# Kernel optimization log

Measured on AMD Instinct MI355X. Metric: run time of the kernel, lower is better.

## Reference

```python
import jax, jax.numpy as jnp
import numpy as np

NTYPES = 2
MAXNEI = 128      # maxNeighborNum
M2 = 16
NPER = 256        # atoms per type
B = 4
EMB = [25, 50, 100]
FIT_IN = M2 * EMB[-1]  # 1600
FH = 240


def setup_inputs() -> dict:
    key = jax.random.key(0)
    ks = jax.random.split(key, 16)
    s = 0.1
    inp = {
        "Ri": jax.random.normal(ks[0], (B, NTYPES * NPER, NTYPES * MAXNEI, 4), jnp.float32),
        "emb_W0": jax.random.normal(ks[1], (4, 1, EMB[0]), jnp.float32) * s,
        "emb_b0": jax.random.normal(ks[2], (4, EMB[0]), jnp.float32) * s,
        "emb_W1": jax.random.normal(ks[3], (4, EMB[0], EMB[1]), jnp.float32) * s,
        "emb_b1": jax.random.normal(ks[4], (4, EMB[1]), jnp.float32) * s,
        "emb_W2": jax.random.normal(ks[5], (4, EMB[1], EMB[2]), jnp.float32) * s,
        "emb_b2": jax.random.normal(ks[6], (4, EMB[2]), jnp.float32) * s,
        "fit_W0": jax.random.normal(ks[7], (2, FIT_IN, FH), jnp.float32) * 0.02,
        "fit_b0": jax.random.normal(ks[8], (2, FH), jnp.float32) * s,
        "fit_W1": jax.random.normal(ks[9], (2, FH, FH), jnp.float32) * 0.05,
        "fit_b1": jax.random.normal(ks[10], (2, FH), jnp.float32) * s,
        "fit_W2": jax.random.normal(ks[11], (2, FH, FH), jnp.float32) * 0.05,
        "fit_b2": jax.random.normal(ks[12], (2, FH), jnp.float32) * s,
        "fit_W3": jax.random.normal(ks[13], (2, FH, 1), jnp.float32) * 0.05,
        "fit_b3": jax.random.normal(ks[14], (2, 1), jnp.float32),
    }
    return inp


def _emb(s, W0, b0, W1, b1, W2, b2):
    # DeepMD-style embedding MLP with doubling resnet skips (1->25->50->100)
    h0 = jnp.tanh(s @ W0 + b0)
    h1 = jnp.tanh(h0 @ W1 + b1) + jnp.concatenate([h0, h0], axis=-1)
    h2 = jnp.tanh(h1 @ W2 + b2) + jnp.concatenate([h1, h1], axis=-1)
    return h2


def _fit(d, W0, b0, W1, b1, W2, b2, W3, b3):
    h = jnp.tanh(d @ W0 + b0)
    h = jnp.tanh(h @ W1 + b1) + h   # resnet skip (equal dims)
    h = jnp.tanh(h @ W2 + b2) + h
    return h @ W3 + b3              # [B, N, 1]


def reference(Ri, emb_W0, emb_b0, emb_W1, emb_b1, emb_W2, emb_b2,
              fit_W0, fit_b0, fit_W1, fit_b1, fit_W2, fit_b2, fit_W3, fit_b3):
    type_nums = NTYPES
    Ei_blocks = []
    for i in range(NTYPES):                      # center-atom type
        Ri_i = Ri[:, i * NPER:(i + 1) * NPER]    # [B, NPER, NTYPES*M, 4]
        xyz = None
        for j in range(NTYPES):                  # neighbor type
            blk = Ri_i[:, :, j * MAXNEI:(j + 1) * MAXNEI, :]  # [B,N,M,4]
            S = blk[..., 0:1]                                  # [B,N,M,1]
            e = i * NTYPES + j
            G = _emb(S, emb_W0[e], emb_b0[e], emb_W1[e], emb_b1[e],
                     emb_W2[e], emb_b2[e])                     # [B,N,M,100]
            tmp = jnp.einsum('bnmc,bnmg->bncg', blk, G)        # [B,N,4,100]
            xyz = tmp if xyz is None else xyz + tmp
        xyz = xyz / (MAXNEI * type_nums)
        xyz_b = xyz[..., :M2]                                  # [B,N,4,16]
        DR = jnp.einsum('bncg,bnch->bngh', xyz, xyz_b)         # [B,N,100,16]
        DR = DR.reshape(B, NPER, FIT_IN)
        Ei_i = _fit(DR, fit_W0[i], fit_b0[i], fit_W1[i], fit_b1[i],
                    fit_W2[i], fit_b2[i], fit_W3[i], fit_b3[i])  # [B,N,1]
        Ei_blocks.append(Ei_i)
    Ei = jnp.concatenate(Ei_blocks, axis=1)     # [B, natoms_sum, 1]
    return Ei[..., 0]                            # per-atom energies [B, natoms_sum]
```

## Files before the change

kernel.cpp:

```cpp
#include <hip/hip_runtime.h>
#include <hip/hip_bf16.h>

#define FH 240
#define FIT_IN 1600
#define NK 2048
#define TLO -16.0f
#define TINVH 64.0f

typedef _Float16 h8 __attribute__((ext_vector_type(8)));
typedef float f4v __attribute__((ext_vector_type(4)));

__device__ __forceinline__ float fast_tanh(float x) {
    float e2 = __builtin_amdgcn_exp2f(x * 2.8853900817779268f);
    return 1.0f - 2.0f * __builtin_amdgcn_rcpf(e2 + 1.0f);
}

#define FMA_ROW(r, s) \
    acc[r][0] += (s) * b0.x; acc[r][1] += (s) * b0.y; \
    acc[r][2] += (s) * b0.z; acc[r][3] += (s) * b0.w; \
    acc[r][4] += (s) * b1.x; acc[r][5] += (s) * b1.y; \
    acc[r][6] += (s) * b1.z; acc[r][7] += (s) * b1.w;

#define TOFF_W0   0
#define TOFF_B0   28
#define TOFF_B1   56
#define TOFF_B2   108
#define TOFF_W1   208
#define TOFF_W2   1508
#define TOFF_H0T  6708
#define TOFF_H1T  10008
#define TSMEM     16608

__global__ __launch_bounds__(256) void k_table(
    const float* __restrict__ eW0, const float* __restrict__ eB0,
    const float* __restrict__ eW1, const float* __restrict__ eB1,
    const float* __restrict__ eW2, const float* __restrict__ eB2,
    float* __restrict__ T)
{
    __shared__ float sm[TSMEM];

    const int t    = threadIdx.x;
    const int w    = t >> 6;
    const int lane = t & 63;
    const int mi   = lane & 7;
    const int gi   = lane >> 3;
    const int mrow = w * 32 + mi * 4;

    const int e  = blockIdx.y;
    const int k0 = blockIdx.x * 128;

    for (int idx = t; idx < 1250; idx += 256) {
        int k = idx / 50, g = idx - k * 50;
        sm[TOFF_W1 + k * 52 + g] = eW1[e * 1250 + idx];
    }
    for (int idx = t; idx < 5000; idx += 256) {
        int k = idx / 100, r = idx - k * 100;
        int half = r / 50, g = r - half * 50;
        sm[TOFF_W2 + k * 104 + half * 52 + g] = eW2[e * 5000 + idx];
    }
    if (t < 25)       { sm[TOFF_W0 + t] = eW0[e * 25 + t]; sm[TOFF_B0 + t] = eB0[e * 25 + t]; }
    else if (t < 75)  { sm[TOFF_B1 + (t - 25)] = eB1[e * 50 + (t - 25)]; }
    else if (t < 175) { sm[TOFF_B2 + (t - 75)] = eB2[e * 100 + (t - 75)]; }
    __syncthreads();

    if (t < 128) {
        const float S = TLO + (float)(k0 + t) * (1.0f / TINVH);
        #pragma unroll
        for (int k = 0; k < 25; ++k)
            sm[TOFF_H0T + k * 132 + t] = fast_tanh(S * sm[TOFF_W0 + k] + sm[TOFF_B0 + k]);
    }
    __syncthreads();

    {
        float acc[4][8];
        #pragma unroll
        for (int r = 0; r < 4; ++r)
            #pragma unroll
            for (int c = 0; c < 8; ++c) acc[r][c] = 0.f;

        #pragma unroll 5
        for (int k = 0; k < 25; ++k) {
            const float4 av = *(const float4*)&sm[TOFF_H0T + k * 132 + mrow];
            const float4 b0 = *(const float4*)&sm[TOFF_W1 + k * 52 + gi * 8];
            const float4 b1 = *(const float4*)&sm[TOFF_W1 + k * 52 + gi * 8 + 4];
            FMA_ROW(0, av.x) FMA_ROW(1, av.y) FMA_ROW(2, av.z) FMA_ROW(3, av.w)
        }
        #pragma unroll
        for (int c = 0; c < 8; ++c) {
            const int g = gi * 8 + c;
            if (g < 50) {
                const int gm = (g < 25) ? g : g - 25;
                const float4 h0r = *(const float4*)&sm[TOFF_H0T + gm * 132 + mrow];
                const float bias = sm[TOFF_B1 + g];
                float4 o;
                o.x = fast_tanh(acc[0][c] + bias) + h0r.x;
                o.y = fast_tanh(acc[1][c] + bias) + h0r.y;
                o.z = fast_tanh(acc[2][c] + bias) + h0r.z;
                o.w = fast_tanh(acc[3][c] + bias) + h0r.w;
                *(float4*)&sm[TOFF_H1T + g * 132 + mrow] = o;
            }
        }
    }
    __syncthreads();

    for (int half = 0; half < 2; ++half) {
        float acc[4][8];
        #pragma unroll
        for (int r = 0; r < 4; ++r)
            #pragma unroll
            for (int c = 0; c < 8; ++c) acc[r][c] = 0.f;

        #pragma unroll 5
        for (int k = 0; k < 50; ++k) {
            const float4 av = *(const float4*)&sm[TOFF_H1T + k * 132 + mrow];
            const float4 b0 = *(const float4*)&sm[TOFF_W2 + k * 104 + half * 52 + gi * 8];
            const float4 b1 = *(const float4*)&sm[TOFF_W2 + k * 104 + half * 52 + gi * 8 + 4];
            FMA_ROW(0, av.x) FMA_ROW(1, av.y) FMA_ROW(2, av.z) FMA_ROW(3, av.w)
        }
        #pragma unroll
        for (int c = 0; c < 8; ++c) {
            const int g = gi * 8 + c;
            if (g < 50) {
                const float4 h1r = *(const float4*)&sm[TOFF_H1T + g * 132 + mrow];
                const float bias = sm[TOFF_B2 + half * 50 + g];
                float* out = T + ((size_t)e * NK + k0 + mrow) * 100 + half * 50 + g;
                out[0]   = fast_tanh(acc[0][c] + bias) + h1r.x;
                out[100] = fast_tanh(acc[1][c] + bias) + h1r.y;
                out[200] = fast_tanh(acc[2][c] + bias) + h1r.z;
                out[300] = fast_tanh(acc[3][c] + bias) + h1r.w;
            }
        }
    }
}

__global__ __launch_bounds__(256) void k_cvt(
    const float* __restrict__ fW0, const float* __restrict__ fW1,
    const float* __restrict__ fW2,
    _Float16* __restrict__ W0T, _Float16* __restrict__ W1T,
    _Float16* __restrict__ W2T)
{
    const int total = 768000 + 115200 + 115200;
    for (int idx = blockIdx.x * 256 + threadIdx.x; idx < total; idx += gridDim.x * 256) {
        if (idx < 768000) {
            const int tp = idx / 384000, r = idx - tp * 384000;
            const int n = r / 1600, k = r - n * 1600;
            W0T[idx] = (_Float16)fW0[tp * 384000 + k * 240 + n];
        } else if (idx < 883200) {
            const int j = idx - 768000;
            const int tp = j / 57600, r = j - tp * 57600;
            const int n = r / 240, k = r - n * 240;
            W1T[j] = (_Float16)fW1[tp * 57600 + k * 240 + n];
        } else {
            const int j = idx - 883200;
            const int tp = j / 57600, r = j - tp * 57600;
            const int n = r / 240, k = r - n * 240;
            W2T[j] = (_Float16)fW2[tp * 57600 + k * 240 + n];
        }
    }
}

__global__ __launch_bounds__(256) void k_xyz(
    const float* __restrict__ Ri, const float* __restrict__ T,
    _Float16* __restrict__ DRh)
{
    __shared__ float4 sR[256];
    __shared__ float  sF[256];
    __shared__ int    sI[256];
    __shared__ float  sXYZ[400];

    const int t   = threadIdx.x;
    const int blk = blockIdx.x;
    const int b   = blk >> 9;
    const int i   = (blk >> 8) & 1;
    const int n   = blk & 255;

    for (int idx = t; idx < 400; idx += 256) sXYZ[idx] = 0.f;

    {
        const int jj = t >> 7, m = t & 127;
        const size_t row = ((size_t)(b * 512 + i * 256 + n)) * 256 + jj * 128 + m;
        const float4 r = *(const float4*)(Ri + row * 4);
        sR[t] = r;
        float u = (r.x - TLO) * TINVH;
        int ii = (int)u;
        ii = (ii < 0) ? 0 : ((ii > NK - 2) ? NK - 2 : ii);
        sI[t] = ii;
        sF[t] = u - (float)ii;
    }
    __syncthreads();

    const int jj = t >> 7;
    const int g  = t & 127;
    if (g < 100) {
        const float* Te = T + ((size_t)(i * 2 + jj)) * NK * 100 + g;
        float a0 = 0.f, a1 = 0.f, a2 = 0.f, a3 = 0.f;
        #pragma unroll 4
        for (int m = 0; m < 128; ++m) {
            const int s = jj * 128 + m;
            const float4 R = sR[s];
            const float  f = sF[s];
            const float* p = Te + (size_t)sI[s] * 100;
            const float v0 = p[0], v1 = p[100];
            const float G = v0 + f * (v1 - v0);
            a0 += R.x * G; a1 += R.y * G; a2 += R.z * G; a3 += R.w * G;
        }
        atomicAdd(&sXYZ[g],       a0);
        atomicAdd(&sXYZ[100 + g], a1);
        atomicAdd(&sXYZ[200 + g], a2);
        atomicAdd(&sXYZ[300 + g], a3);
    }
    __syncthreads();

    const float inv = 1.0f / 65536.0f;
    _Float16* dr = DRh + (((size_t)i * 4 + b) * 256 + n) * FIT_IN;
    for (int q = t; q < 400; q += 256) {
        const int gg = q >> 2, h0 = (q & 3) * 4;
        ushort4 pk;
        _Float16* ph = (_Float16*)&pk;
        #pragma unroll
        for (int r = 0; r < 4; ++r) {
            const int h = h0 + r;
            const float v = (sXYZ[gg] * sXYZ[h] + sXYZ[100 + gg] * sXYZ[100 + h]
                           + sXYZ[200 + gg] * sXYZ[200 + h] + sXYZ[300 + gg] * sXYZ[300 + h]) * inv;
            ph[r] = (_Float16)v;
        }
        *(ushort4*)(dr + gg * 16 + h0) = pk;
    }
}

template<int K, int CHUNK>
__global__ __launch_bounds__(256) void k_fit_mfma(
    const _Float16* __restrict__ A, const _Float16* __restrict__ WT,
    float* __restrict__ P)
{
    __shared__ _Float16 sA[64 * 40];
    __shared__ _Float16 sBT[240 * 40];

    const int t    = threadIdx.x;
    const int w    = t >> 6;
    const int lane = t & 63;
    const int ln   = lane & 15;
    const int quad = lane >> 4;

    const int mtile = blockIdx.x;
    const int ks    = blockIdx.y;
    const int row0  = mtile * 64;
    const int tp    = mtile >> 4;
    const int kbeg  = ks * CHUNK;
    const int kend  = (kbeg + CHUNK < K) ? (kbeg + CHUNK) : K;
    const int nf0   = w * 4;
    const int nfrags = (w < 3) ? 4 : 3;

    f4v acc[4][4];
    #pragma unroll
    for (int mf = 0; mf < 4; ++mf)
        #pragma unroll
        for (int nf = 0; nf < 4; ++nf) acc[mf][nf] = (f4v)0.f;

    const _Float16* Ab = A + (size_t)row0 * K;
    const _Float16* Wb = WT + (size_t)tp * 240 * K;

    for (int k0 = kbeg; k0 < kend; k0 += 32) {
        #pragma unroll
        for (int q = t; q < 512; q += 256) {
            const int m = q >> 3, kq = (q & 7) * 4;
            const int k = k0 + kq;
            uint2 v = make_uint2(0u, 0u);
            if (k < kend) v = *(const uint2*)(Ab + (size_t)m * K + k);
            *(uint2*)&sA[m * 40 + kq] = v;
        }
        for (int q = t; q < 1920; q += 256) {
            const int n = q >> 3, kq = (q & 7) * 4;
            const int k = k0 + kq;
            uint2 v = make_uint2(0u, 0u);
            if (k < kend) v = *(const uint2*)(Wb + (size_t)n * K + k);
            *(uint2*)&sBT[n * 40 + kq] = v;
        }
        __syncthreads();

        h8 afr[4];
        #pragma unroll
        for (int mf = 0; mf < 4; ++mf)
            afr[mf] = *(const h8*)&sA[(mf * 16 + ln) * 40 + quad * 8];
        #pragma unroll
        for (int nf = 0; nf < 4; ++nf) {
            if (nf < nfrags) {
                const h8 bfr = *(const h8*)&sBT[((nf0 + nf) * 16 + ln) * 40 + quad * 8];
                #pragma unroll
                for (int mf = 0; mf < 4; ++mf)
                    acc[mf][nf] = __builtin_amdgcn_mfma_f32_16x16x32_f16(
                        afr[mf], bfr, acc[mf][nf], 0, 0, 0);
            }
        }
        __syncthreads();
    }

    float* Pb = P + ((size_t)ks * 2048 + row0) * FH;
    #pragma unroll
    for (int nf = 0; nf < 4; ++nf) {
        if (nf < nfrags) {
            const int col = (nf0 + nf) * 16 + ln;
            #pragma unroll
            for (int mf = 0; mf < 4; ++mf)
                #pragma unroll
                for (int r = 0; r < 4; ++r) {
                    const int row = mf * 16 + quad * 4 + r;
                    Pb[(size_t)row * FH + col] = acc[mf][nf][r];
                }
        }
    }
}

template<int KSPLIT, bool RES>
__global__ __launch_bounds__(256) void k_fit_reduce(
    const float* __restrict__ P, const float* __restrict__ Bias,
    const float* __restrict__ AinF, float* __restrict__ OutF,
    _Float16* __restrict__ OutH)
{
    const int idx = blockIdx.x * 256 + threadIdx.x;
    if (idx >= 2048 * FH) return;
    const int tp  = idx / (1024 * FH);
    const int col = idx % FH;
    float s = 0.f;
    #pragma unroll
    for (int ks = 0; ks < KSPLIT; ++ks)
        s += P[(size_t)ks * 2048 * FH + idx];
    float v = fast_tanh(s + Bias[tp * FH + col]);
    if (RES) v += AinF[idx];
    OutF[idx] = v;
    OutH[idx] = (_Float16)v;
}

__global__ __launch_bounds__(256) void k_out(
    const float* __restrict__ Hin, const float* __restrict__ W3,
    const float* __restrict__ b3, float* __restrict__ out)
{
    const int wave = (int)((blockIdx.x * 256 + threadIdx.x) >> 6);
    const int lane = threadIdx.x & 63;
    const int tp = wave >> 10;
    const int rem = wave & 1023;
    const int b = rem >> 8, n = rem & 255;
    const float* h = Hin + (size_t)wave * FH;
    const float* wv = W3 + tp * FH;
    float s = 0.f;
    for (int k = lane; k < FH; k += 64) s += h[k] * wv[k];
    #pragma unroll
    for (int off = 32; off > 0; off >>= 1) s += __shfl_down(s, off);
    if (lane == 0) out[b * 512 + tp * 256 + n] = s + b3[tp];
}

extern "C" void kernel_launch(void* const* d_in, const int* in_sizes, int n_in,
                              void* d_out, int out_size, void* d_ws, size_t ws_size,
                              hipStream_t stream)
{
    const float* Ri  = (const float*)d_in[0];
    const float* eW0 = (const float*)d_in[1];
    const float* eB0 = (const float*)d_in[2];
    const float* eW1 = (const float*)d_in[3];
    const float* eB1 = (const float*)d_in[4];
    const float* eW2 = (const float*)d_in[5];
    const float* eB2 = (const float*)d_in[6];
    const float* fW0 = (const float*)d_in[7];
    const float* fb0 = (const float*)d_in[8];
    const float* fW1 = (const float*)d_in[9];
    const float* fb1 = (const float*)d_in[10];
    const float* fW2 = (const float*)d_in[11];
    const float* fb2 = (const float*)d_in[12];
    const float* fW3 = (const float*)d_in[13];
    const float* fb3 = (const float*)d_in[14];

    char* p = (char*)d_ws;
    float* T   = (float*)p;                 p += (size_t)4 * NK * 100 * 4;
    float* P   = (float*)p;                 p += (size_t)17 * 2048 * FH * 4;
    float* hA  = (float*)p;                 p += (size_t)2048 * FH * 4;
    float* hB  = (float*)p;                 p += (size_t)2048 * FH * 4;
    _Float16* DRh = (_Float16*)p;           p += (size_t)2048 * FIT_IN * 2;
    _Float16* hAh = (_Float16*)p;           p += (size_t)2048 * FH * 2;
    _Float16* hBh = (_Float16*)p;           p += (size_t)2048 * FH * 2;
    _Float16* W0T = (_Float16*)p;           p += (size_t)768000 * 2;
    _Float16* W1T = (_Float16*)p;           p += (size_t)115200 * 2;
    _Float16* W2T = (_Float16*)p;           p += (size_t)115200 * 2;

    const int RBLK = (2048 * FH + 255) / 256;

    k_cvt<<<dim3(1024), dim3(256), 0, stream>>>(fW0, fW1, fW2, W0T, W1T, W2T);
    k_table<<<dim3(NK / 128, 4), dim3(256), 0, stream>>>(eW0, eB0, eW1, eB1, eW2, eB2, T);
    k_xyz<<<dim3(2048), dim3(256), 0, stream>>>(Ri, T, DRh);

    k_fit_mfma<FIT_IN, 96><<<dim3(32, 17), dim3(256), 0, stream>>>(DRh, W0T, P);
    k_fit_reduce<17, false><<<dim3(RBLK), dim3(256), 0, stream>>>(P, fb0, nullptr, hA, hAh);

    k_fit_mfma<FH, 32><<<dim3(32, 8), dim3(256), 0, stream>>>(hAh, W1T, P);
    k_fit_reduce<8, true><<<dim3(RBLK), dim3(256), 0, stream>>>(P, fb1, hA, hB, hBh);

    k_fit_mfma<FH, 32><<<dim3(32, 8), dim3(256), 0, stream>>>(hBh, W2T, P);
    k_fit_reduce<8, true><<<dim3(RBLK), dim3(256), 0, stream>>>(P, fb2, hB, hA, hAh);

    k_out<<<dim3(512), dim3(256), 0, stream>>>(hA, fW3, fb3, (float*)d_out);
}
```

Baseline: 196.9 us.

## Fuse prep kernels, restructure xyz gather, and fuse fitting layers with epilogues

The weight-conversion and embedding-table kernels are merged into one launch, and the conversion now reads coalesced and writes scattered. The xyz accumulation is reorganised so each wave handles a slice of neighbours with lanes over embedding channels, giving coalesced table reads across lanes. The first fitting GEMM uses 32-row tiles with an 8-way K split. The two hidden-layer GEMMs become single-pass kernels that apply bias, tanh and the residual in the epilogue, and the last one also computes the output dot product. Together these remove several launches and the split-K partial-sum round trips, at the cost of smaller tiles and fewer blocks in the fused layers.

```diff
diff --git a/kernel.cpp b/kernel.cpp
--- a/kernel.cpp
+++ b/kernel.cpp
@@ -31,23 +31,50 @@
 #define TOFF_H1T  10008
 #define TSMEM     16608
 
-__global__ __launch_bounds__(256) void k_table(
+__global__ __launch_bounds__(256) void k_prep(
     const float* __restrict__ eW0, const float* __restrict__ eB0,
     const float* __restrict__ eW1, const float* __restrict__ eB1,
     const float* __restrict__ eW2, const float* __restrict__ eB2,
-    float* __restrict__ T)
-{
+    float* __restrict__ T,
+    const float* __restrict__ fW0, const float* __restrict__ fW1,
+    const float* __restrict__ fW2,
+    _Float16* __restrict__ W0T, _Float16* __restrict__ W1T,
+    _Float16* __restrict__ W2T)
+{
+    const int bx = blockIdx.x;
+    const int t  = threadIdx.x;
+
+    if (bx >= 64) {
+        const int total = 768000 + 115200 + 115200;
+        for (int idx = (bx - 64) * 256 + t; idx < total; idx += 64 * 256) {
+            if (idx < 768000) {
+                const int tp = idx / 384000, r = idx - tp * 384000;
+                const int k = r / 240, n = r - k * 240;
+                W0T[tp * 384000 + n * 1600 + k] = (_Float16)fW0[idx];
+            } else if (idx < 883200) {
+                const int j = idx - 768000;
+                const int tp = j / 57600, r = j - tp * 57600;
+                const int k = r / 240, n = r - k * 240;
+                W1T[tp * 57600 + n * 240 + k] = (_Float16)fW1[j];
+            } else {
+                const int j = idx - 883200;
+                const int tp = j / 57600, r = j - tp * 57600;
+                const int k = r / 240, n = r - k * 240;
+                W2T[tp * 57600 + n * 240 + k] = (_Float16)fW2[j];
+            }
+        }
+        return;
+    }
+
     __shared__ float sm[TSMEM];
-
-    const int t    = threadIdx.x;
     const int w    = t >> 6;
     const int lane = t & 63;
     const int mi   = lane & 7;
     const int gi   = lane >> 3;
     const int mrow = w * 32 + mi * 4;
 
-    const int e  = blockIdx.y;
-    const int k0 = blockIdx.x * 128;
+    const int e  = bx >> 4;
+    const int k0 = (bx & 15) * 128;
 
     for (int idx = t; idx < 1250; idx += 256) {
         int k = idx / 50, g = idx - k * 50;
@@ -133,32 +160,6 @@
     }
 }
 
-__global__ __launch_bounds__(256) void k_cvt(
-    const float* __restrict__ fW0, const float* __restrict__ fW1,
-    const float* __restrict__ fW2,
-    _Float16* __restrict__ W0T, _Float16* __restrict__ W1T,
-    _Float16* __restrict__ W2T)
-{
-    const int total = 768000 + 115200 + 115200;
-    for (int idx = blockIdx.x * 256 + threadIdx.x; idx < total; idx += gridDim.x * 256) {
-        if (idx < 768000) {
-            const int tp = idx / 384000, r = idx - tp * 384000;
-            const int n = r / 1600, k = r - n * 1600;
-            W0T[idx] = (_Float16)fW0[tp * 384000 + k * 240 + n];
-        } else if (idx < 883200) {
-            const int j = idx - 768000;
-            const int tp = j / 57600, r = j - tp * 57600;
-            const int n = r / 240, k = r - n * 240;
-            W1T[j] = (_Float16)fW1[tp * 57600 + k * 240 + n];
-        } else {
-            const int j = idx - 883200;
-            const int tp = j / 57600, r = j - tp * 57600;
-            const int n = r / 240, k = r - n * 240;
-            W2T[j] = (_Float16)fW2[tp * 57600 + k * 240 + n];
-        }
-    }
-}
-
 __global__ __launch_bounds__(256) void k_xyz(
     const float* __restrict__ Ri, const float* __restrict__ T,
     _Float16* __restrict__ DRh)
@@ -168,11 +169,13 @@
     __shared__ int    sI[256];
     __shared__ float  sXYZ[400];
 
-    const int t   = threadIdx.x;
-    const int blk = blockIdx.x;
-    const int b   = blk >> 9;
-    const int i   = (blk >> 8) & 1;
-    const int n   = blk & 255;
+    const int t    = threadIdx.x;
+    const int w    = t >> 6;
+    const int lane = t & 63;
+    const int blk  = blockIdx.x;
+    const int b    = blk >> 9;
+    const int i    = (blk >> 8) & 1;
+    const int n    = blk & 255;
 
     for (int idx = t; idx < 400; idx += 256) sXYZ[idx] = 0.f;
 
@@ -189,25 +192,34 @@
     }
     __syncthreads();
 
-    const int jj = t >> 7;
-    const int g  = t & 127;
-    if (g < 100) {
-        const float* Te = T + ((size_t)(i * 2 + jj)) * NK * 100 + g;
-        float a0 = 0.f, a1 = 0.f, a2 = 0.f, a3 = 0.f;
+    float a0[4] = {0.f, 0.f, 0.f, 0.f};
+    float a1[4] = {0.f, 0.f, 0.f, 0.f};
+
+    for (int jj = 0; jj < 2; ++jj) {
+        const float* Te = T + (size_t)(i * 2 + jj) * NK * 100;
         #pragma unroll 4
-        for (int m = 0; m < 128; ++m) {
-            const int s = jj * 128 + m;
+        for (int mm = 0; mm < 32; ++mm) {
+            const int s = jj * 128 + (w << 5) + mm;
+            const int row = sI[s];
+            const float f = sF[s];
             const float4 R = sR[s];
-            const float  f = sF[s];
-            const float* p = Te + (size_t)sI[s] * 100;
-            const float v0 = p[0], v1 = p[100];
+            const float* p = Te + (size_t)row * 100;
+            const float v0 = p[lane], v1 = p[100 + lane];
             const float G = v0 + f * (v1 - v0);
-            a0 += R.x * G; a1 += R.y * G; a2 += R.z * G; a3 += R.w * G;
-        }
-        atomicAdd(&sXYZ[g],       a0);
-        atomicAdd(&sXYZ[100 + g], a1);
-        atomicAdd(&sXYZ[200 + g], a2);
-        atomicAdd(&sXYZ[300 + g], a3);
+            a0[0] += R.x * G; a0[1] += R.y * G; a0[2] += R.z * G; a0[3] += R.w * G;
+            if (lane < 36) {
+                const float u0 = p[64 + lane], u1 = p[164 + lane];
+                const float G2 = u0 + f * (u1 - u0);
+                a1[0] += R.x * G2; a1[1] += R.y * G2; a1[2] += R.z * G2; a1[3] += R.w * G2;
+            }
+        }
+    }
+
+    #pragma unroll
+    for (int c = 0; c < 4; ++c) atomicAdd(&sXYZ[c * 100 + lane], a0[c]);
+    if (lane < 36) {
+        #pragma unroll
+        for (int c = 0; c < 4; ++c) atomicAdd(&sXYZ[c * 100 + 64 + lane], a1[c]);
     }
     __syncthreads();
 
@@ -228,12 +240,12 @@
     }
 }
 
-template<int K, int CHUNK>
-__global__ __launch_bounds__(256) void k_fit_mfma(
+__global__ __launch_bounds__(256) void k_fit0(
     const _Float16* __restrict__ A, const _Float16* __restrict__ WT,
     float* __restrict__ P)
 {
-    __shared__ _Float16 sA[64 * 40];
+    constexpr int K = FIT_IN, CHUNK = 200;
+    __shared__ _Float16 sA[32 * 40];
     __shared__ _Float16 sBT[240 * 40];
 
     const int t    = threadIdx.x;
@@ -244,16 +256,14 @@
 
     const int mtile = blockIdx.x;
     const int ks    = blockIdx.y;
-    const int row0  = mtile * 64;
-    const int tp    = mtile >> 4;
-    const int kbeg  = ks * CHUNK;
-    const int kend  = (kbeg + CHUNK < K) ? (kbeg + CHUNK) : K;
+    const int row0  = mtile * 32;
+    const int tp    = mtile >> 5;
+    const int kbeg  = ks * CHUNK, kend = kbeg + CHUNK;
     const int nf0   = w * 4;
-    const int nfrags = (w < 3) ? 4 : 3;
-
-    f4v acc[4][4];
-    #pragma unroll
-    for (int mf = 0; mf < 4; ++mf)
+
+    f4v acc[2][4];
+    #pragma unroll
+    for (int mf = 0; mf < 2; ++mf)
         #pragma unroll
         for (int nf = 0; nf < 4; ++nf) acc[mf][nf] = (f4v)0.f;
 
@@ -261,33 +271,33 @@
     const _Float16* Wb = WT + (size_t)tp * 240 * K;
 
     for (int k0 = kbeg; k0 < kend; k0 += 32) {
-        #pragma unroll
-        for (int q = t; q < 512; q += 256) {
-            const int m = q >> 3, kq = (q & 7) * 4;
+        {
+            const int m = t >> 3, kq = (t & 7) * 4;
             const int k = k0 + kq;
             uint2 v = make_uint2(0u, 0u);
             if (k < kend) v = *(const uint2*)(Ab + (size_t)m * K + k);
             *(uint2*)&sA[m * 40 + kq] = v;
         }
         for (int q = t; q < 1920; q += 256) {
-            const int n = q >> 3, kq = (q & 7) * 4;
+            const int nn = q >> 3, kq = (q & 7) * 4;
             const int k = k0 + kq;
             uint2 v = make_uint2(0u, 0u);
-            if (k < kend) v = *(const uint2*)(Wb + (size_t)n * K + k);
-            *(uint2*)&sBT[n * 40 + kq] = v;
+            if (k < kend) v = *(const uint2*)(Wb + (size_t)nn * K + k);
+            *(uint2*)&sBT[nn * 40 + kq] = v;
         }
         __syncthreads();
 
-        h8 afr[4];
-        #pragma unroll
-        for (int mf = 0; mf < 4; ++mf)
+        h8 afr[2];
+        #pragma unroll
+        for (int mf = 0; mf < 2; ++mf)
             afr[mf] = *(const h8*)&sA[(mf * 16 + ln) * 40 + quad * 8];
         #pragma unroll
         for (int nf = 0; nf < 4; ++nf) {
-            if (nf < nfrags) {
-                const h8 bfr = *(const h8*)&sBT[((nf0 + nf) * 16 + ln) * 40 + quad * 8];
+            const int n15 = nf0 + nf;
+            if (n15 < 15) {
+                const h8 bfr = *(const h8*)&sBT[(n15 * 16 + ln) * 40 + quad * 8];
                 #pragma unroll
-                for (int mf = 0; mf < 4; ++mf)
+                for (int mf = 0; mf < 2; ++mf)
                     acc[mf][nf] = __builtin_amdgcn_mfma_f32_16x16x32_f16(
                         afr[mf], bfr, acc[mf][nf], 0, 0, 0);
             }
@@ -298,24 +308,21 @@
     float* Pb = P + ((size_t)ks * 2048 + row0) * FH;
     #pragma unroll
     for (int nf = 0; nf < 4; ++nf) {
-        if (nf < nfrags) {
-            const int col = (nf0 + nf) * 16 + ln;
+        const int n15 = nf0 + nf;
+        if (n15 < 15) {
+            const int col = n15 * 16 + ln;
             #pragma unroll
-            for (int mf = 0; mf < 4; ++mf)
+            for (int mf = 0; mf < 2; ++mf)
                 #pragma unroll
-                for (int r = 0; r < 4; ++r) {
-                    const int row = mf * 16 + quad * 4 + r;
-                    Pb[(size_t)row * FH + col] = acc[mf][nf][r];
-                }
-        }
-    }
-}
-
-template<int KSPLIT, bool RES>
+                for (int r = 0; r < 4; ++r)
+                    Pb[(size_t)(mf * 16 + quad * 4 + r) * FH + col] = acc[mf][nf][r];
+        }
+    }
+}
+
 __global__ __launch_bounds__(256) void k_fit_reduce(
     const float* __restrict__ P, const float* __restrict__ Bias,
-    const float* __restrict__ AinF, float* __restrict__ OutF,
-    _Float16* __restrict__ OutH)
+    float* __restrict__ OutF, _Float16* __restrict__ OutH)
 {
     const int idx = blockIdx.x * 256 + threadIdx.x;
     if (idx >= 2048 * FH) return;
@@ -323,30 +330,169 @@
     const int col = idx % FH;
     float s = 0.f;
     #pragma unroll
-    for (int ks = 0; ks < KSPLIT; ++ks)
+    for (int ks = 0; ks < 8; ++ks)
         s += P[(size_t)ks * 2048 * FH + idx];
-    float v = fast_tanh(s + Bias[tp * FH + col]);
-    if (RES) v += AinF[idx];
+    const float v = fast_tanh(s + Bias[tp * FH + col]);
     OutF[idx] = v;
     OutH[idx] = (_Float16)v;
 }
 
-__global__ __launch_bounds__(256) void k_out(
-    const float* __restrict__ Hin, const float* __restrict__ W3,
-    const float* __restrict__ b3, float* __restrict__ out)
-{
-    const int wave = (int)((blockIdx.x * 256 + threadIdx.x) >> 6);
-    const int lane = threadIdx.x & 63;
-    const int tp = wave >> 10;
-    const int rem = wave & 1023;
-    const int b = rem >> 8, n = rem & 255;
-    const float* h = Hin + (size_t)wave * FH;
-    const float* wv = W3 + tp * FH;
-    float s = 0.f;
-    for (int k = lane; k < FH; k += 64) s += h[k] * wv[k];
-    #pragma unroll
-    for (int off = 32; off > 0; off >>= 1) s += __shfl_down(s, off);
-    if (lane == 0) out[b * 512 + tp * 256 + n] = s + b3[tp];
+__global__ __launch_bounds__(256) void k_fit_layer(
+    const _Float16* __restrict__ Ah, const _Float16* __restrict__ WT,
+    const float* __restrict__ Bias, const float* __restrict__ ResF,
+    float* __restrict__ OutF, _Float16* __restrict__ OutH)
+{
+    __shared__ _Float16 sA[16 * 264];
+    __shared__ _Float16 sBT[240 * 40];
+
+    const int t    = threadIdx.x;
+    const int w    = t >> 6;
+    const int lane = t & 63;
+    const int ln   = lane & 15;
+    const int quad = lane >> 4;
+
+    const int m0 = blockIdx.x * 16;
+    const int tp = m0 >> 10;
+    const int nf0 = w * 4;
+
+    for (int q = t; q < 1056; q += 256) {
+        const int m = q / 66, kq = (q - m * 66) * 4;
+        uint2 v = make_uint2(0u, 0u);
+        if (kq < 240) v = *(const uint2*)(Ah + (size_t)(m0 + m) * 240 + kq);
+        *(uint2*)&sA[m * 264 + kq] = v;
+    }
+
+    const _Float16* Wb = WT + (size_t)tp * 240 * 240;
+
+    f4v acc[4];
+    #pragma unroll
+    for (int nf = 0; nf < 4; ++nf) acc[nf] = (f4v)0.f;
+
+    for (int k0 = 0; k0 < 240; k0 += 32) {
+        for (int q = t; q < 1920; q += 256) {
+            const int nn = q >> 3, kq = (q & 7) * 4;
+            const int k = k0 + kq;
+            uint2 v = make_uint2(0u, 0u);
+            if (k < 240) v = *(const uint2*)(Wb + (size_t)nn * 240 + k);
+            *(uint2*)&sBT[nn * 40 + kq] = v;
+        }
+        __syncthreads();
+
+        const h8 afr = *(const h8*)&sA[ln * 264 + k0 + quad * 8];
+        #pragma unroll
+        for (int nf = 0; nf < 4; ++nf) {
+            const int n15 = nf0 + nf;
+            if (n15 < 15) {
+                const h8 bfr = *(const h8*)&sBT[(n15 * 16 + ln) * 40 + quad * 8];
+                acc[nf] = __builtin_amdgcn_mfma_f32_16x16x32_f16(afr, bfr, acc[nf], 0, 0, 0);
+            }
+        }
+        __syncthreads();
+    }
+
+    #pragma unroll
+    for (int nf = 0; nf < 4; ++nf) {
+        const int n15 = nf0 + nf;
+        if (n15 < 15) {
+            const int col = n15 * 16 + ln;
+            #pragma unroll
+            for (int r = 0; r < 4; ++r) {
+                const int row = quad * 4 + r;
+                const size_t o = (size_t)(m0 + row) * FH + col;
+                const float v = fast_tanh(acc[nf][r] + Bias[tp * FH + col]) + ResF[o];
+                OutF[o] = v;
+                OutH[o] = (_Float16)v;
+            }
+        }
+    }
+}
+
+__global__ __launch_bounds__(256) void k_fit_last(
+    const _Float16* __restrict__ Ah, const _Float16* __restrict__ WT,
+    const float* __restrict__ Bias, const float* __restrict__ ResF,
+    const float* __restrict__ W3, const float* __restrict__ b3,
+    float* __restrict__ out)
+{
+    __shared__ _Float16 sA[16 * 264];
+    __shared__ _Float16 sBT[240 * 40];
+    __shared__ float sH[16 * 244];
+    __shared__ float sW3[240];
+
+    const int t    = threadIdx.x;
+    const int w    = t >> 6;
+    const int lane = t & 63;
+    const int ln   = lane & 15;
+    const int quad = lane >> 4;
+
+    const int m0 = blockIdx.x * 16;
+    const int tp = m0 >> 10;
+    const int nf0 = w * 4;
+
+    for (int q = t; q < 1056; q += 256) {
+        const int m = q / 66, kq = (q - m * 66) * 4;
+        uint2 v = make_uint2(0u, 0u);
+        if (kq < 240) v = *(const uint2*)(Ah + (size_t)(m0 + m) * 240 + kq);
+        *(uint2*)&sA[m * 264 + kq] = v;
+    }
+    if (t < 240) sW3[t] = W3[tp * 240 + t];
+
+    const _Float16* Wb = WT + (size_t)tp * 240 * 240;
+
+    f4v acc[4];
+    #pragma unroll
+    for (int nf = 0; nf < 4; ++nf) acc[nf] = (f4v)0.f;
+
+    for (int k0 = 0; k0 < 240; k0 += 32) {
+        for (int q = t; q < 1920; q += 256) {
+            const int nn = q >> 3, kq = (q & 7) * 4;
+            const int k = k0 + kq;
+            uint2 v = make_uint2(0u, 0u);
+            if (k < 240) v = *(const uint2*)(Wb + (size_t)nn * 240 + k);
+            *(uint2*)&sBT[nn * 40 + kq] = v;
+        }
+        __syncthreads();
+
+        const h8 afr = *(const h8*)&sA[ln * 264 + k0 + quad * 8];
+        #pragma unroll
+        for (int nf = 0; nf < 4; ++nf) {
+            const int n15 = nf0 + nf;
+            if (n15 < 15) {
+                const h8 bfr = *(const h8*)&sBT[(n15 * 16 + ln) * 40 + quad * 8];
+                acc[nf] = __builtin_amdgcn_mfma_f32_16x16x32_f16(afr, bfr, acc[nf], 0, 0, 0);
+            }
+        }
+        __syncthreads();
+    }
+
+    #pragma unroll
+    for (int nf = 0; nf < 4; ++nf) {
+        const int n15 = nf0 + nf;
+        if (n15 < 15) {
+            const int col = n15 * 16 + ln;
+            #pragma unroll
+            for (int r = 0; r < 4; ++r) {
+                const int row = quad * 4 + r;
+                sH[row * 244 + col] = fast_tanh(acc[nf][r] + Bias[tp * FH + col])
+                                    + ResF[(size_t)(m0 + row) * FH + col];
+            }
+        }
+    }
+    __syncthreads();
+
+    #pragma unroll
+    for (int rr = 0; rr < 4; ++rr) {
+        const int row = w * 4 + rr;
+        float s = 0.f;
+        for (int c = lane; c < 240; c += 64) s += sH[row * 244 + c] * sW3[c];
+        #pragma unroll
+        for (int off = 32; off > 0; off >>= 1) s += __shfl_down(s, off);
+        if (lane == 0) {
+            const int g = m0 + row;
+            const int rem = g & 1023;
+            const int bb = rem >> 8, nn = rem & 255;
+            out[bb * 512 + tp * 256 + nn] = s + b3[tp];
+        }
+    }
 }
 
 extern "C" void kernel_launch(void* const* d_in, const int* in_sizes, int n_in,
@@ -370,31 +516,27 @@
     const float* fb3 = (const float*)d_in[14];
 
     char* p = (char*)d_ws;
-    float* T   = (float*)p;                 p += (size_t)4 * NK * 100 * 4;
-    float* P   = (float*)p;                 p += (size_t)17 * 2048 * FH * 4;
-    float* hA  = (float*)p;                 p += (size_t)2048 * FH * 4;
-    float* hB  = (float*)p;                 p += (size_t)2048 * FH * 4;
-    _Float16* DRh = (_Float16*)p;           p += (size_t)2048 * FIT_IN * 2;
-    _Float16* hAh = (_Float16*)p;           p += (size_t)2048 * FH * 2;
-    _Float16* hBh = (_Float16*)p;           p += (size_t)2048 * FH * 2;
-    _Float16* W0T = (_Float16*)p;           p += (size_t)768000 * 2;
-    _Float16* W1T = (_Float16*)p;           p += (size_t)115200 * 2;
-    _Float16* W2T = (_Float16*)p;           p += (size_t)115200 * 2;
+    float* T      = (float*)p;      p += (size_t)4 * NK * 100 * 4;
+    float* P      = (float*)p;      p += (size_t)8 * 2048 * FH * 4;
+    float* hA     = (float*)p;      p += (size_t)2048 * FH * 4;
+    float* hB     = (float*)p;      p += (size_t)2048 * FH * 4;
+    _Float16* DRh = (_Float16*)p;   p += (size_t)2048 * FIT_IN * 2;
+    _Float16* hAh = (_Float16*)p;   p += (size_t)2048 * FH * 2;
+    _Float16* hBh = (_Float16*)p;   p += (size_t)2048 * FH * 2;
+    _Float16* W0T = (_Float16*)p;   p += (size_t)768000 * 2;
+    _Float16* W1T = (_Float16*)p;   p += (size_t)115200 * 2;
+    _Float16* W2T = (_Float16*)p;   p += (size_t)115200 * 2;
 
     const int RBLK = (2048 * FH + 255) / 256;
 
-    k_cvt<<<dim3(1024), dim3(256), 0, stream>>>(fW0, fW1, fW2, W0T, W1T, W2T);
-    k_table<<<dim3(NK / 128, 4), dim3(256), 0, stream>>>(eW0, eB0, eW1, eB1, eW2, eB2, T);
+    k_prep<<<dim3(128), dim3(256), 0, stream>>>(eW0, eB0, eW1, eB1, eW2, eB2, T,
+                                                fW0, fW1, fW2, W0T, W1T, W2T);
     k_xyz<<<dim3(2048), dim3(256), 0, stream>>>(Ri, T, DRh);
 
-    k_fit_mfma<FIT_IN, 96><<<dim3(32, 17), dim3(256), 0, stream>>>(DRh, W0T, P);
-    k_fit_reduce<17, false><<<dim3(RBLK), dim3(256), 0, stream>>>(P, fb0, nullptr, hA, hAh);
-
-    k_fit_mfma<FH, 32><<<dim3(32, 8), dim3(256), 0, stream>>>(hAh, W1T, P);
-    k_fit_reduce<8, true><<<dim3(RBLK), dim3(256), 0, stream>>>(P, fb1, hA, hB, hBh);
-
-    k_fit_mfma<FH, 32><<<dim3(32, 8), dim3(256), 0, stream>>>(hBh, W2T, P);
-    k_fit_reduce<8, true><<<dim3(RBLK), dim3(256), 0, stream>>>(P, fb2, hB, hA, hAh);
-
-    k_out<<<dim3(512), dim3(256), 0, stream>>>(hA, fW3, fb3, (float*)d_out);
-}
+    k_fit0<<<dim3(64, 8), dim3(256), 0, stream>>>(DRh, W0T, P);
+    k_fit_reduce<<<dim3(RBLK), dim3(256), 0, stream>>>(P, fb0, hA, hAh);
+
+    k_fit_layer<<<dim3(128), dim3(256), 0, stream>>>(hAh, W1T, fb1, hA, hB, hBh);
+    k_fit_last<<<dim3(128), dim3(256), 0, stream>>>(hBh, W2T, fb2, hB, fW3, fb3,
+                                                    (float*)d_out);
+}
```

Measured after the change: 210.9 us. +7.1%, slower.
